# Optimization experiments

Measured on AMD Instinct MI355X. Metric: run time of the kernel, lower is better.

The kernel has to match this reference:

```python
import jax, jax.numpy as jnp
import numpy as np
from jax import lax

_CLIP_MIN = 1e-06
_CLIP_MAX = 1.0
_POS_ALPHA = 0.0005
NUM_CLASSES = 21
RADIUS = 3
HALF_D = RADIUS * RADIUS
POOL = 3
PAD = POOL // 2
IGNORE = 255
LAM = 0.5  # loss_weight_lambda, lambda_way=1


def _max_pool(x):
    # NCHW max pool, kernel=stride=3, padding=1
    return lax.reduce_window(x, -jnp.inf, lax.max,
                             (1, 1, POOL, POOL), (1, 1, POOL, POOL),
                             ((0, 0), (0, 0), (PAD, PAD), (PAD, PAD)))


def _get_pairs(x):
    # stack radius*radius shifted crops -> [N, C, r^2, nh, nw]
    h, w = x.shape[2], x.shape[3]
    nh, nw = h - RADIUS + 1, w - RADIUS + 1
    crops = [x[:, :, y:y + nh, xo:xo + nw] for y in range(RADIUS) for xo in range(RADIUS)]
    return jnp.stack(crops, axis=2)


def _log_det_by_cholesky(m):
    chol = jnp.linalg.cholesky(m)
    return 2.0 * jnp.sum(jnp.log(jnp.diagonal(chol, axis1=-2, axis2=-1) + 1e-08), axis=-1)


def _rmi_lower_bound(labels_4d, probs_4d):
    la = _max_pool(labels_4d)
    pr = _max_pool(probs_4d)
    n, c = la.shape[0], la.shape[1]
    la_v = _get_pairs(la).reshape(n, c, HALF_D, -1)   # [N,C,d,L]
    pr_v = _get_pairs(pr).reshape(n, c, HALF_D, -1)
    la_v = la_v - jnp.mean(la_v, axis=3, keepdims=True)
    pr_v = pr_v - jnp.mean(pr_v, axis=3, keepdims=True)
    la_cov = jnp.einsum('ncdl,ncel->ncde', la_v, la_v)
    pr_cov = jnp.einsum('ncdl,ncel->ncde', pr_v, pr_v)
    eye = jnp.eye(HALF_D, dtype=la_cov.dtype)
    pr_cov_inv = jnp.linalg.inv(pr_cov + eye * _POS_ALPHA)
    la_pr_cov = jnp.einsum('ncdl,ncel->ncde', la_v, pr_v)
    appro_var = la_cov - jnp.einsum('ncde,ncef,ncgf->ncdg', la_pr_cov, pr_cov_inv, la_pr_cov)
    rmi_now = 0.5 * _log_det_by_cholesky(appro_var + eye * _POS_ALPHA)  # [N,C]
    rmi_per_class = jnp.mean(rmi_now.reshape(-1, NUM_CLASSES), axis=0) / float(HALF_D)
    return jnp.sum(rmi_per_class)


def setup_inputs() -> dict:
    key = jax.random.key(0)
    k1, k2 = jax.random.split(key)
    score = jax.random.normal(k1, (4, NUM_CLASSES, 512, 512), dtype=jnp.float32)
    target = jax.random.randint(k2, (4, 512, 512), 0, NUM_CLASSES, dtype=jnp.int64)
    return {"score": score, "target": target}


def reference(score, target):
    # cross entropy with ignore_index=255, mean reduction
    logp = jax.nn.log_softmax(score, axis=1)                      # [N,C,H,W]
    valid_ce = (target != IGNORE)
    safe_t = jnp.where(valid_ce, target, 0)
    nll = -jnp.take_along_axis(logp, safe_t[:, None].astype(jnp.int32), axis=1)[:, 0]
    normal_loss = jnp.sum(jnp.where(valid_ce, nll, 0.0)) / jnp.sum(valid_ce.astype(jnp.float32))

    # valid one-hot labels and masked sigmoid probs
    mask = (target < NUM_CLASSES)                                 # [N,H,W]
    maskf = mask.astype(jnp.float32)
    onehot = jax.nn.one_hot((target * mask).astype(jnp.int32), NUM_CLASSES, dtype=jnp.float32)
    onehot = onehot * maskf[..., None]                            # [N,H,W,C]
    onehot = jnp.transpose(onehot, (0, 3, 1, 2))                  # [N,C,H,W]
    probs = jnp.clip(jax.nn.sigmoid(score) * maskf[:, None], _CLIP_MIN, _CLIP_MAX)

    rmi_loss = _rmi_lower_bound(onehot, probs)
    return LAM * normal_loss + rmi_loss * (1.0 - LAM)
```

## Files before the change

### kernel.cpp

```cpp
#include <hip/hip_runtime.h>
#include <cfloat>
#include <cmath>

#define DEVINL __device__ __forceinline__

constexpr int N_ = 4, C_ = 21, H_ = 512, W_ = 512;
constexpr int P_ = 171;
constexpr int Q_ = 169;
constexpr int NC_ = N_ * C_;
constexpr int HW_ = H_ * W_;
constexpr int PP_ = 29241;
constexpr int PROW_ = 172;
constexpr int PPAD_ = PROW_ * P_;
constexpr int NCOV_ = 189;
constexpr float EPS_ = 5e-4f;
constexpr int RC_ = 43;
constexpr int G_ = 43;

constexpr int NB_CE = N_ * HW_ / 4 / 256;
constexpr int NB_PL = (NC_ * P_ * G_ + 255) / 256;

typedef float f4_t __attribute__((ext_vector_type(4)));

DEVINL constexpr int tstart(int d) { return d * 9 - d * (d - 1) / 2; }

template <int CTRL>
DEVINL float dpp_add(float v) {
    int x = __builtin_amdgcn_update_dpp(0, __float_as_int(v), CTRL, 0xF, 0xF, false);
    return v + __int_as_float(x);
}

DEVINL float wave_sum63(float v) {
    v = dpp_add<0x111>(v);
    v = dpp_add<0x112>(v);
    v = dpp_add<0x114>(v);
    v = dpp_add<0x118>(v);
    v = dpp_add<0x142>(v);
    v = dpp_add<0x143>(v);
    return v;
}

__global__ __launch_bounds__(256) void k_bits(const int* __restrict__ target,
                                              unsigned* __restrict__ pack) {
    int tid = blockIdx.x * 256 + threadIdx.x;
    if (tid >= N_ * PP_) return;
    int cell = tid % PP_;
    int n = tid / PP_;
    int j = cell % P_;
    int i = cell / P_;
    int hl = 3 * i - 1; if (hl < 0) hl = 0;
    int wl = 3 * j - 1; if (wl < 0) wl = 0;
    int hmax = 3 * i + 1, wmax = 3 * j + 1;
    const int* tb = target + (size_t)n * HW_;
    unsigned oh = 0, px = 0;
#pragma unroll
    for (int r = 0; r < 3; ++r) {
        int hh = hl + r;
        bool hv = hh <= hmax;
        const int* trow = tb + hh * W_;
#pragma unroll
        for (int dc = 0; dc < 3; ++dc) {
            int ww = wl + dc;
            int t = trow[ww];
            if (hv && (ww <= wmax) && t >= 0 && t < C_) {
                oh |= 1u << t;
                px |= 1u << (r * 3 + dc);
            }
        }
    }
    pack[tid] = oh | (px << 23);
}

template <int IDX>
DEVINL void do_cell(const float (&f)[3][16], unsigned pk, int c, float* prp, float* lap) {
    unsigned px = pk >> 23;
    float vm = -FLT_MAX;
#pragma unroll
    for (int r = 0; r < 3; ++r)
#pragma unroll
        for (int dc = 0; dc < 3; ++dc)
            vm = fmaxf(vm, ((px >> (r * 3 + dc)) & 1u) ? f[r][IDX + dc] : -FLT_MAX);
    float p = __builtin_amdgcn_rcpf(1.f + __expf(-vm));
    p = fminf(fmaxf(p, 1e-6f), 1.f);
    *prp = p;
    *lap = ((pk >> c) & 1u) ? 1.f : 0.f;
}

__global__ __launch_bounds__(256) void k_mix(const float* __restrict__ score,
                                             const int* __restrict__ target,
                                             const unsigned* __restrict__ pack,
                                             float* __restrict__ pr,
                                             float* __restrict__ la,
                                             float* __restrict__ cov) {
    int bid = blockIdx.x;
    int t = threadIdx.x;

    if (bid < NB_CE) {
        __shared__ float rn[4], rc[4];
        int tid = bid * 256 + t;
        int p0 = tid * 4;
        int n = p0 >> 18;
        int hw = p0 & (HW_ - 1);
        const float* sp = score + (size_t)n * C_ * HW_ + hw;
        int4 t4 = *(const int4*)(target + p0);

        float4 se = {0.f, 0.f, 0.f, 0.f};
        float4 stgt = {0.f, 0.f, 0.f, 0.f};
        f4_t s[7];
#pragma unroll
        for (int cb = 0; cb < C_; cb += 7) {
#pragma unroll
            for (int u = 0; u < 7; ++u)
                s[u] = *(const f4_t*)(sp + (size_t)(cb + u) * HW_);
            asm volatile("" : "+v"(s[0]), "+v"(s[1]), "+v"(s[2]), "+v"(s[3]),
                              "+v"(s[4]), "+v"(s[5]), "+v"(s[6]));
#pragma unroll
            for (int u = 0; u < 7; ++u) {
                int c = cb + u;
                se.x += __expf(s[u].x);
                se.y += __expf(s[u].y);
                se.z += __expf(s[u].z);
                se.w += __expf(s[u].w);
                if (t4.x == c) stgt.x = s[u].x;
                if (t4.y == c) stgt.y = s[u].y;
                if (t4.z == c) stgt.z = s[u].z;
                if (t4.w == c) stgt.w = s[u].w;
            }
        }
        float nll = 0.f, cnt = 0.f;
        if (t4.x != 255) { nll += __logf(se.x) - stgt.x; cnt += 1.f; }
        if (t4.y != 255) { nll += __logf(se.y) - stgt.y; cnt += 1.f; }
        if (t4.z != 255) { nll += __logf(se.z) - stgt.z; cnt += 1.f; }
        if (t4.w != 255) { nll += __logf(se.w) - stgt.w; cnt += 1.f; }

        nll = wave_sum63(nll);
        cnt = wave_sum63(cnt);
        int wv = t >> 6, lane = t & 63;
        if (lane == 63) { rn[wv] = nll; rc[wv] = cnt; }
        __syncthreads();
        if (t == 0)
            atomicAdd(&cov[NC_ * NCOV_ + 0], rn[0] + rn[1] + rn[2] + rn[3]);
        if (t == 64)
            atomicAdd(&cov[NC_ * NCOV_ + 1], rc[0] + rc[1] + rc[2] + rc[3]);
    } else {
        int tid = (bid - NB_CE) * 256 + t;
        if (tid >= NC_ * P_ * G_) return;
        int g = tid % G_;
        int rest = tid / G_;
        int i = rest % P_;
        int ncidx = rest / P_;
        int n = ncidx / C_;
        int c = ncidx - n * C_;

        int hl = 3 * i - 1; if (hl < 0) hl = 0;
        int b = (g == 0) ? 0 : 12 * g - 4;
        int o3 = (b + 15 < W_) ? 12 : 8;

        const float* sb = score + (size_t)ncidx * HW_ + (size_t)hl * W_ + b;
        float f[3][16];
#pragma unroll
        for (int r = 0; r < 3; ++r) {
            const float* rp = sb + r * W_;
            float4 q0 = *(const float4*)(rp);
            float4 q1 = *(const float4*)(rp + 4);
            float4 q2 = *(const float4*)(rp + 8);
            float4 q3 = *(const float4*)(rp + o3);
            f[r][0] = q0.x;  f[r][1] = q0.y;  f[r][2] = q0.z;  f[r][3] = q0.w;
            f[r][4] = q1.x;  f[r][5] = q1.y;  f[r][6] = q1.z;  f[r][7] = q1.w;
            f[r][8] = q2.x;  f[r][9] = q2.y;  f[r][10] = q2.z; f[r][11] = q2.w;
            f[r][12] = q3.x; f[r][13] = q3.y; f[r][14] = q3.z; f[r][15] = q3.w;
        }

        const unsigned* pkp = pack + n * PP_ + i * P_ + 4 * g;
        size_t ob = (size_t)ncidx * PPAD_ + (size_t)i * PROW_ + 4 * g;
        if (g == 0) {
            do_cell<0>(f, pkp[0], c, pr + ob + 0, la + ob + 0);
            do_cell<2>(f, pkp[1], c, pr + ob + 1, la + ob + 1);
            do_cell<5>(f, pkp[2], c, pr + ob + 2, la + ob + 2);
            do_cell<8>(f, pkp[3], c, pr + ob + 3, la + ob + 3);
        } else {
            do_cell<3>(f, pkp[0], c, pr + ob + 0, la + ob + 0);
            do_cell<6>(f, pkp[1], c, pr + ob + 1, la + ob + 1);
            do_cell<9>(f, pkp[2], c, pr + ob + 2, la + ob + 2);
            if (4 * g + 3 < P_)
                do_cell<12>(f, pkp[3], c, pr + ob + 3, la + ob + 3);
        }
    }
}

template <int D0, int D1>
DEVINL void cov_tri(const float* __restrict__ X, float* __restrict__ cov,
                    int nc, int r0, int rend, int s2base,
                    int tid, float (*red)[27]) {
    constexpr int NS2 = ((9 - D0) * (10 - D0) - (9 - D1) * (10 - D1)) / 2;
    constexpr int RLO = D0 / 3;
    constexpr int KOFF = tstart(D0);
    float s2[NS2];
#pragma unroll
    for (int k = 0; k < NS2; ++k) s2[k] = 0.f;

    int nitems = (rend - r0) * G_;
    for (int idx = tid; idx < nitems; idx += 256) {
        int lr = idx / G_;
        int q = idx - lr * G_;
        int x0 = q * 4;
        const float* base = X + (size_t)(r0 + lr) * PROW_ + x0;
        float v[3][8];
#pragma unroll
        for (int r = RLO; r < 3; ++r) {
            float4 u0 = *(const float4*)(base + r * PROW_);
            float4 u1 = *(const float4*)(base + r * PROW_ + 4);
            v[r][0] = u0.x; v[r][1] = u0.y; v[r][2] = u0.z; v[r][3] = u0.w;
            v[r][4] = u1.x; v[r][5] = u1.y; v[r][6] = u1.z; v[r][7] = u1.w;
        }
#pragma unroll
        for (int p = 0; p < 4; ++p) {
            if (x0 + p < Q_) {
                int k = 0;
#pragma unroll
                for (int d = D0; d < D1; ++d)
#pragma unroll
                    for (int e = d; e < 9; ++e) {
                        s2[k] += v[d / 3][p + d % 3] * v[e / 3][p + e % 3];
                        ++k;
                    }
            }
        }
    }

    int lane = tid & 63, wv = tid >> 6;
#pragma unroll
    for (int k = 0; k < NS2; ++k) {
        float v2 = wave_sum63(s2[k]);
        if (lane == 63) red[wv][k] = v2;
    }
    __syncthreads();
    if (tid < NS2) {
        float v2 = red[0][tid] + red[1][tid] + red[2][tid] + red[3][tid];
        atomicAdd(&cov[nc * NCOV_ + s2base + KOFF + tid], v2);
    }
}

template <int RA>
DEVINL void cov_ab(const float* __restrict__ A, const float* __restrict__ B,
                   float* __restrict__ cov, int nc, int r0, int rend,
                   int tid, float (*red)[27]) {
    float sab[27];
#pragma unroll
    for (int k = 0; k < 27; ++k) sab[k] = 0.f;

    int nitems = (rend - r0) * G_;
    for (int idx = tid; idx < nitems; idx += 256) {
        int lr = idx / G_;
        int q = idx - lr * G_;
        int x0 = q * 4;
        size_t off = (size_t)(r0 + lr) * PROW_ + x0;
        float a[8];
        {
            float4 u0 = *(const float4*)(A + off + RA * PROW_);
            float4 u1 = *(const float4*)(A + off + RA * PROW_ + 4);
            a[0] = u0.x; a[1] = u0.y; a[2] = u0.z; a[3] = u0.w;
            a[4] = u1.x; a[5] = u1.y; a[6] = u1.z; a[7] = u1.w;
        }
#pragma unroll
        for (int r = 0; r < 3; ++r) {
            float b[8];
            {
                float4 w0 = *(const float4*)(B + off + r * PROW_);
                float4 w1 = *(const float4*)(B + off + r * PROW_ + 4);
                b[0] = w0.x; b[1] = w0.y; b[2] = w0.z; b[3] = w0.w;
                b[4] = w1.x; b[5] = w1.y; b[6] = w1.z; b[7] = w1.w;
            }
#pragma unroll
            for (int p = 0; p < 4; ++p) {
                if (x0 + p < Q_) {
#pragma unroll
                    for (int dm = 0; dm < 3; ++dm)
#pragma unroll
                        for (int e2 = 0; e2 < 3; ++e2)
                            sab[dm * 9 + r * 3 + e2] += a[p + dm] * b[p + e2];
                }
            }
        }
    }

    int lane = tid & 63, wv = tid >> 6;
#pragma unroll
    for (int k = 0; k < 27; ++k) {
        float v2 = wave_sum63(sab[k]);
        if (lane == 63) red[wv][k] = v2;
    }
    __syncthreads();
    if (tid < 27) {
        float v2 = red[0][tid] + red[1][tid] + red[2][tid] + red[3][tid];
        atomicAdd(&cov[nc * NCOV_ + 108 + RA * 27 + tid], v2);
    }
}

DEVINL void cov_s1(const float* __restrict__ LA, const float* __restrict__ PR,
                   float* __restrict__ cov, int nc, int r0, int rend,
                   int tid, float (*red)[27]) {
    float s1a[9], s1b[9];
#pragma unroll
    for (int k = 0; k < 9; ++k) { s1a[k] = 0.f; s1b[k] = 0.f; }

    int nitems = (rend - r0) * G_;
    for (int idx = tid; idx < nitems; idx += 256) {
        int lr = idx / G_;
        int q = idx - lr * G_;
        int x0 = q * 4;
        size_t off = (size_t)(r0 + lr) * PROW_ + x0;
#pragma unroll
        for (int r = 0; r < 3; ++r) {
            float va[8], vb[8];
            {
                float4 u0 = *(const float4*)(LA + off + r * PROW_);
                float4 u1 = *(const float4*)(LA + off + r * PROW_ + 4);
                va[0] = u0.x; va[1] = u0.y; va[2] = u0.z; va[3] = u0.w;
                va[4] = u1.x; va[5] = u1.y; va[6] = u1.z; va[7] = u1.w;
                float4 w0 = *(const float4*)(PR + off + r * PROW_);
                float4 w1 = *(const float4*)(PR + off + r * PROW_ + 4);
                vb[0] = w0.x; vb[1] = w0.y; vb[2] = w0.z; vb[3] = w0.w;
                vb[4] = w1.x; vb[5] = w1.y; vb[6] = w1.z; vb[7] = w1.w;
            }
#pragma unroll
            for (int p = 0; p < 4; ++p) {
                if (x0 + p < Q_) {
#pragma unroll
                    for (int dc = 0; dc < 3; ++dc) {
                        s1a[r * 3 + dc] += va[p + dc];
                        s1b[r * 3 + dc] += vb[p + dc];
                    }
                }
            }
        }
    }

    int lane = tid & 63, wv = tid >> 6;
#pragma unroll
    for (int k = 0; k < 9; ++k) {
        float v2 = wave_sum63(s1a[k]);
        if (lane == 63) red[wv][k] = v2;
    }
#pragma unroll
    for (int k = 0; k < 9; ++k) {
        float v2 = wave_sum63(s1b[k]);
        if (lane == 63) red[wv][9 + k] = v2;
    }
    __syncthreads();
    if (tid < 18) {
        float v2 = red[0][tid] + red[1][tid] + red[2][tid] + red[3][tid];
        atomicAdd(&cov[nc * NCOV_ + tid], v2);
    }
}

__global__ __launch_bounds__(256) void k_cov(const float* __restrict__ la,
                                             const float* __restrict__ pr,
                                             float* __restrict__ cov) {
    __shared__ float red[4][27];
    int nc = blockIdx.x;
    int chunk = blockIdx.y;
    int part = blockIdx.z;
    int r0 = chunk * RC_;
    int rend = r0 + RC_;
    if (rend > Q_) rend = Q_;
    int tid = threadIdx.x;
    const float* LA = la + (size_t)nc * PPAD_;
    const float* PR = pr + (size_t)nc * PPAD_;

    switch (part) {
        case 0: cov_tri<0, 3>(LA, cov, nc, r0, rend, 18, tid, red); break;
        case 1: cov_tri<3, 9>(LA, cov, nc, r0, rend, 18, tid, red); break;
        case 2: cov_tri<0, 3>(PR, cov, nc, r0, rend, 63, tid, red); break;
        case 3: cov_tri<3, 9>(PR, cov, nc, r0, rend, 63, tid, red); break;
        case 4: cov_ab<0>(LA, PR, cov, nc, r0, rend, tid, red); break;
        case 5: cov_ab<1>(LA, PR, cov, nc, r0, rend, tid, red); break;
        case 6: cov_ab<2>(LA, PR, cov, nc, r0, rend, tid, red); break;
        case 7: cov_s1(LA, PR, cov, nc, r0, rend, tid, red); break;
    }
}

__global__ __launch_bounds__(128) void k_final(const float* __restrict__ cov,
                                               float* __restrict__ out) {
    __shared__ float red[128];
    int t = threadIdx.x;
    float my = 0.f;
    if (t < NC_) {
        const float* S = cov + t * NCOV_;
        const float Lf = (float)(Q_ * Q_);
        float sA[9], sB[9];
#pragma unroll
        for (int d = 0; d < 9; ++d) { sA[d] = S[d]; sB[d] = S[9 + d]; }
        float laC[45], M[45], Cm[81];
        {
            int k = 0;
#pragma unroll
            for (int d = 0; d < 9; ++d)
#pragma unroll
                for (int e = d; e < 9; ++e) {
                    laC[k] = S[18 + k] - sA[d] * sA[e] / Lf;
                    M[k] = S[63 + k] - sB[d] * sB[e] / Lf + (d == e ? EPS_ : 0.f);
                    ++k;
                }
#pragma unroll
            for (int d = 0; d < 9; ++d)
#pragma unroll
                for (int e = 0; e < 9; ++e)
                    Cm[d * 9 + e] = S[108 + d * 9 + e] - sA[d] * sB[e] / Lf;
        }
#pragma unroll
        for (int j = 0; j < 9; ++j) {
            float s = M[tstart(j)];
#pragma unroll
            for (int k = 0; k < j; ++k) { float l = M[tstart(k) + (j - k)]; s -= l * l; }
            float dj = sqrtf(fmaxf(s, 1e-30f));
            M[tstart(j)] = dj;
            float inv = 1.f / dj;
#pragma unroll
            for (int i = j + 1; i < 9; ++i) {
                float s2 = M[tstart(j) + (i - j)];
#pragma unroll
                for (int k = 0; k < j; ++k)
                    s2 -= M[tstart(k) + (i - k)] * M[tstart(k) + (j - k)];
                M[tstart(j) + (i - j)] = s2 * inv;
            }
        }
#pragma unroll
        for (int p = 0; p < 9; ++p) {
#pragma unroll
            for (int i = 0; i < 9; ++i) {
                float s = Cm[p * 9 + i];
#pragma unroll
                for (int k = 0; k < i; ++k)
                    s -= M[tstart(k) + (i - k)] * Cm[p * 9 + k];
                Cm[p * 9 + i] = s / M[tstart(i)];
            }
        }
#pragma unroll
        for (int d = 0; d < 9; ++d)
#pragma unroll
            for (int e = d; e < 9; ++e) {
                float s = 0.f;
#pragma unroll
                for (int i = 0; i < 9; ++i) s += Cm[d * 9 + i] * Cm[e * 9 + i];
                laC[tstart(d) + (e - d)] -= s;
                if (d == e) laC[tstart(d)] += EPS_;
            }
        float rmi = 0.f;
#pragma unroll
        for (int j = 0; j < 9; ++j) {
            float s = laC[tstart(j)];
#pragma unroll
            for (int k = 0; k < j; ++k) { float l = laC[tstart(k) + (j - k)]; s -= l * l; }
            float dj = sqrtf(fmaxf(s, 0.f));
            laC[tstart(j)] = dj;
            float inv = 1.f / fmaxf(dj, 1e-30f);
#pragma unroll
            for (int i = j + 1; i < 9; ++i) {
                float s2 = laC[tstart(j) + (i - j)];
#pragma unroll
                for (int k = 0; k < j; ++k)
                    s2 -= laC[tstart(k) + (i - k)] * laC[tstart(k) + (j - k)];
                laC[tstart(j) + (i - j)] = s2 * inv;
            }
            rmi += __logf(dj + 1e-8f);
        }
        my = rmi;
    }
    red[t] = my;
    __syncthreads();
#pragma unroll
    for (int o = 64; o > 0; o >>= 1) {
        if (t < o) red[t] += red[t + o];
        __syncthreads();
    }
    if (t == 0) {
        float rmi_total = red[0] / 36.f;
        float ce = cov[NC_ * NCOV_ + 0] / cov[NC_ * NCOV_ + 1];
        out[0] = 0.5f * ce + 0.5f * rmi_total;
    }
}

extern "C" void kernel_launch(void* const* d_in, const int* in_sizes, int n_in,
                              void* d_out, int out_size, void* d_ws, size_t ws_size,
                              hipStream_t stream) {
    const float* score = (const float*)d_in[0];
    const int* target = (const int*)d_in[1];
    float* pr = (float*)d_ws;
    float* la = pr + (size_t)NC_ * PPAD_;
    float* cov = la + (size_t)NC_ * PPAD_;
    unsigned* pack = (unsigned*)(cov + NC_ * NCOV_ + 2);
    hipMemsetAsync(cov, 0, (size_t)(NC_ * NCOV_ + 2) * sizeof(float), stream);

    k_bits<<<dim3((N_ * PP_ + 255) / 256), dim3(256), 0, stream>>>(target, pack);
    k_mix<<<dim3(NB_CE + NB_PL), dim3(256), 0, stream>>>(score, target, pack, pr, la, cov);
    k_cov<<<dim3(NC_, 4, 8), dim3(256), 0, stream>>>(la, pr, cov);
    k_final<<<dim3(1), dim3(128), 0, stream>>>(cov, (float*)d_out);
}
```

Baseline: 254.2 us.

## Fuse target bit-packing into mix kernel, stagger CE channel loads, widen padded row

Removes the separate k_bits launch and its pack buffer. Each pooling thread now recomputes the one-hot and valid-pixel bitmasks for its four cells straight from target. The CE branch rotates which 7-channel block each wave loads first, using a per-block/wave phase, to spread memory accesses across channel planes, and keeps per-block partial sums so the summation order stays fixed. The padded pooled row stride grows from 172 to 192, presumably for alignment in k_cov. The cost is redundant target reads, since every channel recomputes the same bits, about 21x more target loads.

```diff
diff --git a/kernel.cpp b/kernel.cpp
--- a/kernel.cpp
+++ b/kernel.cpp
@@ -9,8 +9,7 @@
 constexpr int Q_ = 169;
 constexpr int NC_ = N_ * C_;
 constexpr int HW_ = H_ * W_;
-constexpr int PP_ = 29241;
-constexpr int PROW_ = 172;
+constexpr int PROW_ = 192;
 constexpr int PPAD_ = PROW_ * P_;
 constexpr int NCOV_ = 189;
 constexpr float EPS_ = 5e-4f;
@@ -40,18 +39,10 @@
     return v;
 }
 
-__global__ __launch_bounds__(256) void k_bits(const int* __restrict__ target,
-                                              unsigned* __restrict__ pack) {
-    int tid = blockIdx.x * 256 + threadIdx.x;
-    if (tid >= N_ * PP_) return;
-    int cell = tid % PP_;
-    int n = tid / PP_;
-    int j = cell % P_;
-    int i = cell / P_;
+DEVINL unsigned bits_cell(const int* __restrict__ tb, int i, int j) {
     int hl = 3 * i - 1; if (hl < 0) hl = 0;
     int wl = 3 * j - 1; if (wl < 0) wl = 0;
     int hmax = 3 * i + 1, wmax = 3 * j + 1;
-    const int* tb = target + (size_t)n * HW_;
     unsigned oh = 0, px = 0;
 #pragma unroll
     for (int r = 0; r < 3; ++r) {
@@ -68,7 +59,7 @@
             }
         }
     }
-    pack[tid] = oh | (px << 23);
+    return oh | (px << 23);
 }
 
 template <int IDX>
@@ -88,12 +79,12 @@
 
 __global__ __launch_bounds__(256) void k_mix(const float* __restrict__ score,
                                              const int* __restrict__ target,
-                                             const unsigned* __restrict__ pack,
                                              float* __restrict__ pr,
                                              float* __restrict__ la,
                                              float* __restrict__ cov) {
     int bid = blockIdx.x;
     int t = threadIdx.x;
+    int wv = t >> 6, lane = t & 63;
 
     if (bid < NB_CE) {
         __shared__ float rn[4], rc[4];
@@ -104,29 +95,42 @@
         const float* sp = score + (size_t)n * C_ * HW_ + hw;
         int4 t4 = *(const int4*)(target + p0);
 
-        float4 se = {0.f, 0.f, 0.f, 0.f};
+        float4 se0 = {0.f, 0.f, 0.f, 0.f}, se1 = se0, se2 = se0;
         float4 stgt = {0.f, 0.f, 0.f, 0.f};
+        int phase = (bid + wv) % 3;
         f4_t s[7];
 #pragma unroll
-        for (int cb = 0; cb < C_; cb += 7) {
+        for (int kk = 0; kk < 3; ++kk) {
+            int b = kk + phase; if (b >= 3) b -= 3;
+            int cb = b * 7;
 #pragma unroll
             for (int u = 0; u < 7; ++u)
                 s[u] = *(const f4_t*)(sp + (size_t)(cb + u) * HW_);
             asm volatile("" : "+v"(s[0]), "+v"(s[1]), "+v"(s[2]), "+v"(s[3]),
                               "+v"(s[4]), "+v"(s[5]), "+v"(s[6]));
+            float4 acc = {0.f, 0.f, 0.f, 0.f};
 #pragma unroll
             for (int u = 0; u < 7; ++u) {
                 int c = cb + u;
-                se.x += __expf(s[u].x);
-                se.y += __expf(s[u].y);
-                se.z += __expf(s[u].z);
-                se.w += __expf(s[u].w);
+                acc.x += __expf(s[u].x);
+                acc.y += __expf(s[u].y);
+                acc.z += __expf(s[u].z);
+                acc.w += __expf(s[u].w);
                 if (t4.x == c) stgt.x = s[u].x;
                 if (t4.y == c) stgt.y = s[u].y;
                 if (t4.z == c) stgt.z = s[u].z;
                 if (t4.w == c) stgt.w = s[u].w;
             }
-        }
+            if (b == 0) se0 = acc;
+            else if (b == 1) se1 = acc;
+            else se2 = acc;
+        }
+        float4 se;
+        se.x = (se0.x + se1.x) + se2.x;
+        se.y = (se0.y + se1.y) + se2.y;
+        se.z = (se0.z + se1.z) + se2.z;
+        se.w = (se0.w + se1.w) + se2.w;
+
         float nll = 0.f, cnt = 0.f;
         if (t4.x != 255) { nll += __logf(se.x) - stgt.x; cnt += 1.f; }
         if (t4.y != 255) { nll += __logf(se.y) - stgt.y; cnt += 1.f; }
@@ -135,7 +139,6 @@
 
         nll = wave_sum63(nll);
         cnt = wave_sum63(cnt);
-        int wv = t >> 6, lane = t & 63;
         if (lane == 63) { rn[wv] = nll; rc[wv] = cnt; }
         __syncthreads();
         if (t == 0)
@@ -152,6 +155,12 @@
         int n = ncidx / C_;
         int c = ncidx - n * C_;
 
+        const int* tb = target + (size_t)n * HW_;
+        unsigned pk0 = bits_cell(tb, i, 4 * g + 0);
+        unsigned pk1 = bits_cell(tb, i, 4 * g + 1);
+        unsigned pk2 = bits_cell(tb, i, 4 * g + 2);
+        unsigned pk3 = (4 * g + 3 < P_) ? bits_cell(tb, i, 4 * g + 3) : 0u;
+
         int hl = 3 * i - 1; if (hl < 0) hl = 0;
         int b = (g == 0) ? 0 : 12 * g - 4;
         int o3 = (b + 15 < W_) ? 12 : 8;
@@ -171,19 +180,18 @@
             f[r][12] = q3.x; f[r][13] = q3.y; f[r][14] = q3.z; f[r][15] = q3.w;
         }
 
-        const unsigned* pkp = pack + n * PP_ + i * P_ + 4 * g;
         size_t ob = (size_t)ncidx * PPAD_ + (size_t)i * PROW_ + 4 * g;
         if (g == 0) {
-            do_cell<0>(f, pkp[0], c, pr + ob + 0, la + ob + 0);
-            do_cell<2>(f, pkp[1], c, pr + ob + 1, la + ob + 1);
-            do_cell<5>(f, pkp[2], c, pr + ob + 2, la + ob + 2);
-            do_cell<8>(f, pkp[3], c, pr + ob + 3, la + ob + 3);
+            do_cell<0>(f, pk0, c, pr + ob + 0, la + ob + 0);
+            do_cell<2>(f, pk1, c, pr + ob + 1, la + ob + 1);
+            do_cell<5>(f, pk2, c, pr + ob + 2, la + ob + 2);
+            do_cell<8>(f, pk3, c, pr + ob + 3, la + ob + 3);
         } else {
-            do_cell<3>(f, pkp[0], c, pr + ob + 0, la + ob + 0);
-            do_cell<6>(f, pkp[1], c, pr + ob + 1, la + ob + 1);
-            do_cell<9>(f, pkp[2], c, pr + ob + 2, la + ob + 2);
+            do_cell<3>(f, pk0, c, pr + ob + 0, la + ob + 0);
+            do_cell<6>(f, pk1, c, pr + ob + 1, la + ob + 1);
+            do_cell<9>(f, pk2, c, pr + ob + 2, la + ob + 2);
             if (4 * g + 3 < P_)
-                do_cell<12>(f, pkp[3], c, pr + ob + 3, la + ob + 3);
+                do_cell<12>(f, pk3, c, pr + ob + 3, la + ob + 3);
         }
     }
 }
@@ -489,11 +497,9 @@
     float* pr = (float*)d_ws;
     float* la = pr + (size_t)NC_ * PPAD_;
     float* cov = la + (size_t)NC_ * PPAD_;
-    unsigned* pack = (unsigned*)(cov + NC_ * NCOV_ + 2);
     hipMemsetAsync(cov, 0, (size_t)(NC_ * NCOV_ + 2) * sizeof(float), stream);
 
-    k_bits<<<dim3((N_ * PP_ + 255) / 256), dim3(256), 0, stream>>>(target, pack);
-    k_mix<<<dim3(NB_CE + NB_PL), dim3(256), 0, stream>>>(score, target, pack, pr, la, cov);
+    k_mix<<<dim3(NB_CE + NB_PL), dim3(256), 0, stream>>>(score, target, pr, la, cov);
     k_cov<<<dim3(NC_, 4, 8), dim3(256), 0, stream>>>(la, pr, cov);
     k_final<<<dim3(1), dim3(128), 0, stream>>>(cov, (float*)d_out);
 }
```

Result: no change. 256.9 us (+1.0%).

## Stage CE score loads through LDS via global_load_lds, fold memset into k_bits

Applied to the files above, without the earlier changes.

The cross-entropy branch of k_mix now streams score channels into shared memory with direct global-to-LDS loads, seven channels per phase, followed by a wait and a barrier before reading them back. The hipMemsetAsync of the accumulator buffer is removed and the zeroing moves into block 0 of k_bits, saving one launch. The padded row stride PROW_ grows from 172 to 192, which likely aligns rows for the k_cov path. The new path adds shared memory use and extra barriers per phase, which may reduce occupancy and overlap compared with register-held loads.

```diff
diff --git a/kernel.cpp b/kernel.cpp
--- a/kernel.cpp
+++ b/kernel.cpp
@@ -10,7 +10,7 @@
 constexpr int NC_ = N_ * C_;
 constexpr int HW_ = H_ * W_;
 constexpr int PP_ = 29241;
-constexpr int PROW_ = 172;
+constexpr int PROW_ = 192;
 constexpr int PPAD_ = PROW_ * P_;
 constexpr int NCOV_ = 189;
 constexpr float EPS_ = 5e-4f;
@@ -21,6 +21,8 @@
 constexpr int NB_PL = (NC_ * P_ * G_ + 255) / 256;
 
 typedef float f4_t __attribute__((ext_vector_type(4)));
+typedef __attribute__((address_space(1))) const void gas_void;
+typedef __attribute__((address_space(3))) void las_void;
 
 DEVINL constexpr int tstart(int d) { return d * 9 - d * (d - 1) / 2; }
 
@@ -41,8 +43,13 @@
 }
 
 __global__ __launch_bounds__(256) void k_bits(const int* __restrict__ target,
-                                              unsigned* __restrict__ pack) {
-    int tid = blockIdx.x * 256 + threadIdx.x;
+                                              unsigned* __restrict__ pack,
+                                              float* __restrict__ cov) {
+    int t = threadIdx.x;
+    if (blockIdx.x == 0) {
+        for (int k = t; k < NC_ * NCOV_ + 2; k += 256) cov[k] = 0.f;
+    }
+    int tid = blockIdx.x * 256 + t;
     if (tid >= N_ * PP_) return;
     int cell = tid % PP_;
     int n = tid / PP_;
@@ -61,9 +68,9 @@
 #pragma unroll
         for (int dc = 0; dc < 3; ++dc) {
             int ww = wl + dc;
-            int t = trow[ww];
-            if (hv && (ww <= wmax) && t >= 0 && t < C_) {
-                oh |= 1u << t;
+            int tv = trow[ww];
+            if (hv && (ww <= wmax) && tv >= 0 && tv < C_) {
+                oh |= 1u << tv;
                 px |= 1u << (r * 3 + dc);
             }
         }
@@ -92,41 +99,48 @@
                                              float* __restrict__ pr,
                                              float* __restrict__ la,
                                              float* __restrict__ cov) {
+    __shared__ float lds[7 * 1024];
+    __shared__ float rn[4], rc[4];
     int bid = blockIdx.x;
     int t = threadIdx.x;
+    int wv = t >> 6, lane = t & 63;
 
     if (bid < NB_CE) {
-        __shared__ float rn[4], rc[4];
-        int tid = bid * 256 + t;
-        int p0 = tid * 4;
-        int n = p0 >> 18;
-        int hw = p0 & (HW_ - 1);
-        const float* sp = score + (size_t)n * C_ * HW_ + hw;
+        int n = bid >> 8;
+        int bhw = (bid * 1024) & (HW_ - 1);
+        const float* sp0 = score + (size_t)n * C_ * HW_ + bhw;
+        int p0 = bid * 1024 + t * 4;
         int4 t4 = *(const int4*)(target + p0);
 
         float4 se = {0.f, 0.f, 0.f, 0.f};
         float4 stgt = {0.f, 0.f, 0.f, 0.f};
-        f4_t s[7];
-#pragma unroll
-        for (int cb = 0; cb < C_; cb += 7) {
-#pragma unroll
-            for (int u = 0; u < 7; ++u)
-                s[u] = *(const f4_t*)(sp + (size_t)(cb + u) * HW_);
-            asm volatile("" : "+v"(s[0]), "+v"(s[1]), "+v"(s[2]), "+v"(s[3]),
-                              "+v"(s[4]), "+v"(s[5]), "+v"(s[6]));
+        for (int ph = 0; ph < 3; ++ph) {
 #pragma unroll
             for (int u = 0; u < 7; ++u) {
-                int c = cb + u;
-                se.x += __expf(s[u].x);
-                se.y += __expf(s[u].y);
-                se.z += __expf(s[u].z);
-                se.w += __expf(s[u].w);
-                if (t4.x == c) stgt.x = s[u].x;
-                if (t4.y == c) stgt.y = s[u].y;
-                if (t4.z == c) stgt.z = s[u].z;
-                if (t4.w == c) stgt.w = s[u].w;
-            }
-        }
+                int c = ph * 7 + u;
+                const float* g = sp0 + (size_t)c * HW_ + t * 4;
+                float* l = &lds[u * 1024 + wv * 256];
+                __builtin_amdgcn_global_load_lds((gas_void*)g, (las_void*)l,
+                                                 16, 0, 0);
+            }
+            asm volatile("s_waitcnt vmcnt(0)" ::: "memory");
+            __syncthreads();
+#pragma unroll
+            for (int u = 0; u < 7; ++u) {
+                int c = ph * 7 + u;
+                f4_t v = *(const f4_t*)&lds[u * 1024 + t * 4];
+                se.x += __expf(v.x);
+                se.y += __expf(v.y);
+                se.z += __expf(v.z);
+                se.w += __expf(v.w);
+                if (t4.x == c) stgt.x = v.x;
+                if (t4.y == c) stgt.y = v.y;
+                if (t4.z == c) stgt.z = v.z;
+                if (t4.w == c) stgt.w = v.w;
+            }
+            __syncthreads();
+        }
+
         float nll = 0.f, cnt = 0.f;
         if (t4.x != 255) { nll += __logf(se.x) - stgt.x; cnt += 1.f; }
         if (t4.y != 255) { nll += __logf(se.y) - stgt.y; cnt += 1.f; }
@@ -135,7 +149,6 @@
 
         nll = wave_sum63(nll);
         cnt = wave_sum63(cnt);
-        int wv = t >> 6, lane = t & 63;
         if (lane == 63) { rn[wv] = nll; rc[wv] = cnt; }
         __syncthreads();
         if (t == 0)
@@ -490,9 +503,8 @@
     float* la = pr + (size_t)NC_ * PPAD_;
     float* cov = la + (size_t)NC_ * PPAD_;
     unsigned* pack = (unsigned*)(cov + NC_ * NCOV_ + 2);
-    hipMemsetAsync(cov, 0, (size_t)(NC_ * NCOV_ + 2) * sizeof(float), stream);
-
-    k_bits<<<dim3((N_ * PP_ + 255) / 256), dim3(256), 0, stream>>>(target, pack);
+
+    k_bits<<<dim3((N_ * PP_ + 255) / 256), dim3(256), 0, stream>>>(target, pack, cov);
     k_mix<<<dim3(NB_CE + NB_PL), dim3(256), 0, stream>>>(score, target, pack, pr, la, cov);
     k_cov<<<dim3(NC_, 4, 8), dim3(256), 0, stream>>>(la, pr, cov);
     k_final<<<dim3(1), dim3(128), 0, stream>>>(cov, (float*)d_out);
```

After: 251.1 us. About the same (-1.2%).
